# Kernel optimization log

Measured on AMD Instinct MI355X. Metric: run time of the kernel, lower is better.

Reference implementation:

```python
import jax, jax.numpy as jnp
import numpy as np

GRID_LO = 32
GRID_HI = 128
NF = 4          # n_features
K = 9           # num_neighbors
NUM_CLASSES = 36
BS = 128
P_LO = GRID_LO * GRID_LO   # 1024
P_HI = GRID_HI * GRID_HI   # 16384


def _knn_neighbor_indices():
    """Replicates cKDTree(lo_coords).query(hi_coords, k=K)[1]: lo grid has
    spacing ratio=grid_hi//grid_lo, hi grid spacing 1; neighbors sorted by
    distance (stable sort -> ties broken by lower linear index)."""
    ratio = GRID_HI // GRID_LO
    lo = np.stack(np.meshgrid(np.arange(GRID_LO) * ratio,
                              np.arange(GRID_LO) * ratio, indexing='ij'),
                  axis=-1).reshape(-1, 2).astype(np.float64)   # (P_LO, 2)
    hi = np.stack(np.meshgrid(np.arange(GRID_HI),
                              np.arange(GRID_HI), indexing='ij'),
                  axis=-1).reshape(-1, 2).astype(np.float64)   # (P_HI, 2)
    d2 = ((hi[:, None, :] - lo[None, :, :]) ** 2).sum(-1)      # (P_HI, P_LO)
    idx = np.argsort(d2, axis=1, kind='stable')[:, :K]          # (P_HI, K)
    return jnp.asarray(idx, dtype=jnp.int32)


def setup_inputs() -> dict:
    key = jax.random.key(0)
    k1, k2, k3, k4, k5 = jax.random.split(key, 5)
    x = jax.random.normal(k1, (BS, NF * P_LO), dtype=jnp.float32)
    cls_ids = jax.random.randint(k2, (BS,), 0, NUM_CLASSES)
    neighbor_indices = _knn_neighbor_indices()                  # (P_HI, K)
    weight_map = jax.random.normal(k3, (NUM_CLASSES, NF, P_HI, K), dtype=jnp.float32) * 0.05
    bias_low = jax.random.normal(k4, (NUM_CLASSES, NF, P_LO), dtype=jnp.float32) * 0.05
    bias_high = jax.random.normal(k5, (NUM_CLASSES, NF, P_HI), dtype=jnp.float32) * 0.05
    return {"x": x, "cls_ids": cls_ids, "neighbor_indices": neighbor_indices,
            "weight_map": weight_map, "bias_low": bias_low, "bias_high": bias_high}


def reference(x, cls_ids, neighbor_indices, weight_map, bias_low, bias_high):
    # x: (BS, NF*P_LO) -> (BS, NF, P_LO)
    y_low = x.reshape(x.shape[0], NF, P_LO)
    y_low_db = y_low - bias_low[cls_ids]                        # (BS, NF, P_LO)
    # gather k=9 lo-res neighbors for every hi-res pixel (all features at once)
    neigh = y_low_db[:, :, neighbor_indices]                    # (BS, NF, P_HI, K)
    weights = weight_map[cls_ids]                               # (BS, NF, P_HI, K)
    out = jnp.einsum('bfpk,bfpk->bfp', neigh, weights)          # weighted sum over k
    out = out + bias_high[cls_ids]                              # (BS, NF, P_HI)
    return out.reshape(x.shape[0], NF, GRID_HI, GRID_HI)
```

## Files before the change

kernel.cpp:

```cpp
#include <hip/hip_runtime.h>

#define BS      128
#define NF      4
#define NC      36
#define P_LO    1024
#define P_HI    16384
#define KNN     9
#define THREADS 256
#define TILE_P  256
#define NTILES  (P_HI / TILE_P)
#define LIST_OFF 64

__global__ __launch_bounds__(128) void build_lists_kernel(
    const int* __restrict__ cls_ids, int* __restrict__ ws)
{
    __shared__ int cnt[NC];
    const int t = threadIdx.x;
    if (t < NC) cnt[t] = 0;
    __syncthreads();
    if (t < BS) {
        int c = cls_ids[t];
        int pos = atomicAdd(&cnt[c], 1);
        ws[LIST_OFF + c * BS + pos] = t;
    }
    __syncthreads();
    if (t < NC) ws[t] = cnt[t];
}

__device__ __forceinline__ void async_cp16(const void* g, void* l) {
    __builtin_amdgcn_global_load_lds(
        (const __attribute__((address_space(1))) void*)g,
        (__attribute__((address_space(3))) void*)l, 16, 0, 0);
}

__global__ __launch_bounds__(THREADS) void rect_up_kernel(
    const float* __restrict__ x,
    const int*   __restrict__ ws,
    const int*   __restrict__ nbr,
    const float* __restrict__ wmap,
    const float* __restrict__ blo,
    const float* __restrict__ bhi,
    float*       __restrict__ out)
{
    __shared__ __align__(16) char smem[2 * TILE_P * KNN * 4];

    const int tile = blockIdx.x % NTILES;
    const int cf   = blockIdx.x / NTILES;
    const int f    = cf % NF;
    const int cls  = cf / NF;

    const int n_b = ws[cls];
    if (n_b == 0) return;

    const int tid   = threadIdx.x;
    const int tbase = tile * TILE_P;
    const int p     = tbase + tid;

    const float4* wsrc = (const float4*)(wmap + ((size_t)(cls * NF + f) * P_HI + tbase) * KNN);
    const float4* isrc = (const float4*)(nbr + (size_t)tbase * KNN);
    float4* wdst = (float4*)smem;
    float4* idst = (float4*)(smem + TILE_P * KNN * 4);
    async_cp16(wsrc + tid,       wdst + tid);
    async_cp16(wsrc + tid + 256, wdst + tid + 256);
    async_cp16(isrc + tid,       idst + tid);
    async_cp16(isrc + tid + 256, idst + tid + 256);
    if (tid < 64) {
        async_cp16(wsrc + 512 + tid, wdst + 512 + tid);
        async_cp16(isrc + 512 + tid, idst + 512 + tid);
    }

    const float* blp = blo + (size_t)(cls * NF + f) * P_LO;
    float blv0 = blp[tid];
    float blv1 = blp[tid + 256];
    float blv2 = blp[tid + 512];
    float blv3 = blp[tid + 768];
    const float bh = bhi[(size_t)(cls * NF + f) * P_HI + p];
    const int* list = ws + LIST_OFF + cls * BS;

    asm volatile("s_waitcnt vmcnt(0)" ::: "memory");
    __syncthreads();

    float w[KNN]; int nb[KNN];
    {
        const float* wrow = (const float*)smem + (size_t)tid * KNN;
        const int*   irow = (const int*)(smem + TILE_P * KNN * 4) + (size_t)tid * KNN;
        #pragma unroll
        for (int k = 0; k < KNN; ++k) { w[k] = wrow[k]; nb[k] = irow[k]; }
    }
    __syncthreads();

    float4* ybuf = (float4*)smem;

    const int R = (n_b + 3) >> 2;
    for (int r = 0; r < R; ++r) {
        const int s0 = 4 * r;
        const int b0 = list[s0];
        const int b1 = list[(s0 + 1 < n_b) ? s0 + 1 : n_b - 1];
        const int b2 = list[(s0 + 2 < n_b) ? s0 + 2 : n_b - 1];
        const int b3 = list[(s0 + 3 < n_b) ? s0 + 3 : n_b - 1];
        const float* x0 = x + ((size_t)(b0 * NF + f)) * P_LO;
        const float* x1 = x + ((size_t)(b1 * NF + f)) * P_LO;
        const float* x2 = x + ((size_t)(b2 * NF + f)) * P_LO;
        const float* x3 = x + ((size_t)(b3 * NF + f)) * P_LO;

        if (r) __syncthreads();

        {
            float blv[4] = {blv0, blv1, blv2, blv3};
            #pragma unroll
            for (int m = 0; m < 4; ++m) {
                const int q = tid + (m << 8);
                const float bl = blv[m];
                float4 v;
                v.x = x0[q] - bl;
                v.y = x1[q] - bl;
                v.z = x2[q] - bl;
                v.w = x3[q] - bl;
                ybuf[q] = v;
            }
        }
        __syncthreads();

        float a0 = 0.f, a1 = 0.f, a2 = 0.f, a3 = 0.f;
        #pragma unroll
        for (int k = 0; k < KNN; ++k) {
            const float4 yv = ybuf[nb[k]];
            a0 = fmaf(w[k], yv.x, a0);
            a1 = fmaf(w[k], yv.y, a1);
            a2 = fmaf(w[k], yv.z, a2);
            a3 = fmaf(w[k], yv.w, a3);
        }

        out[(size_t)(b0 * NF + f) * P_HI + p] = a0 + bh;
        if (s0 + 1 < n_b) out[(size_t)(b1 * NF + f) * P_HI + p] = a1 + bh;
        if (s0 + 2 < n_b) out[(size_t)(b2 * NF + f) * P_HI + p] = a2 + bh;
        if (s0 + 3 < n_b) out[(size_t)(b3 * NF + f) * P_HI + p] = a3 + bh;
    }
}

extern "C" void kernel_launch(void* const* d_in, const int* in_sizes, int n_in,
                              void* d_out, int out_size, void* d_ws, size_t ws_size,
                              hipStream_t stream) {
    const float* x    = (const float*)d_in[0];
    const int*   cls  = (const int*)d_in[1];
    const int*   nbr  = (const int*)d_in[2];
    const float* wmap = (const float*)d_in[3];
    const float* blo  = (const float*)d_in[4];
    const float* bhi  = (const float*)d_in[5];
    float*       out  = (float*)d_out;
    int*         wsl  = (int*)d_ws;

    build_lists_kernel<<<1, 128, 0, stream>>>(cls, wsl);
    rect_up_kernel<<<NC * NF * NTILES, THREADS, 0, stream>>>(
        x, wsl, nbr, wmap, blo, bhi, out);
}
```

Baseline: 158.1 us.

## Loop features inside each block, prefetch next feature weights, schedule heavy classes first

Each block now handles all four features for one class and tile instead of one feature, so the neighbor-index tile is loaded once and reused across features. The next feature's weights and first x rows are prefetched asynchronously while the current feature computes. The list-building kernel also sorts classes by batch count so that blocks for the most populated classes launch first, reducing tail imbalance. This cuts the grid by a factor of four and raises per-block serial work, and it also increases register use for the prefetched x values.

```diff
diff --git a/kernel.cpp b/kernel.cpp
--- a/kernel.cpp
+++ b/kernel.cpp
@@ -10,13 +10,19 @@
 #define TILE_P  256
 #define NTILES  (P_HI / TILE_P)
 #define LIST_OFF 64
+#define SCHED_OFF 36
+
+#define WBUF_BYTES (TILE_P * KNN * 4)
+#define YBUF_BYTES (P_LO * 16)
 
 __global__ __launch_bounds__(128) void build_lists_kernel(
     const int* __restrict__ cls_ids, int* __restrict__ ws)
 {
     __shared__ int cnt[NC];
+    __shared__ int pk[9];
     const int t = threadIdx.x;
     if (t < NC) cnt[t] = 0;
+    if (t >= 64 && t < 73) pk[t - 64] = 0;
     __syncthreads();
     if (t < BS) {
         int c = cls_ids[t];
@@ -24,7 +30,18 @@
         ws[LIST_OFF + c * BS + pos] = t;
     }
     __syncthreads();
-    if (t < NC) ws[t] = cnt[t];
+    if (t < NC) {
+        int ct = cnt[t];
+        ws[t] = ct;
+        int r = 0;
+        for (int j = 0; j < NC; ++j) {
+            int cj = cnt[j];
+            r += (cj > ct) || (cj == ct && j < t);
+        }
+        atomicOr(&pk[r >> 2], t << ((r & 3) << 3));
+    }
+    __syncthreads();
+    if (t < 9) ws[SCHED_OFF + t] = pk[t];
 }
 
 __device__ __forceinline__ void async_cp16(const void* g, void* l) {
@@ -42,12 +59,11 @@
     const float* __restrict__ bhi,
     float*       __restrict__ out)
 {
-    __shared__ __align__(16) char smem[2 * TILE_P * KNN * 4];
-
-    const int tile = blockIdx.x % NTILES;
-    const int cf   = blockIdx.x / NTILES;
-    const int f    = cf % NF;
-    const int cls  = cf / NF;
+    __shared__ __align__(16) char smem[WBUF_BYTES + YBUF_BYTES];
+
+    const int tile = blockIdx.x & (NTILES - 1);
+    const int g    = blockIdx.x >> 6;
+    const int cls  = (ws[SCHED_OFF + (g >> 2)] >> ((g & 3) << 3)) & 0xFF;
 
     const int n_b = ws[cls];
     if (n_b == 0) return;
@@ -56,85 +72,147 @@
     const int tbase = tile * TILE_P;
     const int p     = tbase + tid;
 
-    const float4* wsrc = (const float4*)(wmap + ((size_t)(cls * NF + f) * P_HI + tbase) * KNN);
-    const float4* isrc = (const float4*)(nbr + (size_t)tbase * KNN);
-    float4* wdst = (float4*)smem;
-    float4* idst = (float4*)(smem + TILE_P * KNN * 4);
-    async_cp16(wsrc + tid,       wdst + tid);
-    async_cp16(wsrc + tid + 256, wdst + tid + 256);
-    async_cp16(isrc + tid,       idst + tid);
-    async_cp16(isrc + tid + 256, idst + tid + 256);
-    if (tid < 64) {
-        async_cp16(wsrc + 512 + tid, wdst + 512 + tid);
-        async_cp16(isrc + 512 + tid, idst + 512 + tid);
-    }
-
-    const float* blp = blo + (size_t)(cls * NF + f) * P_LO;
-    float blv0 = blp[tid];
-    float blv1 = blp[tid + 256];
-    float blv2 = blp[tid + 512];
-    float blv3 = blp[tid + 768];
-    const float bh = bhi[(size_t)(cls * NF + f) * P_HI + p];
+    float4* wbuf  = (float4*)smem;
+    float4* ybuf4 = (float4*)(smem + WBUF_BYTES);
+    float4* idst  = ybuf4;
+
+    {
+        const float4* wsrc = (const float4*)(wmap + ((size_t)(cls * NF + 0) * P_HI + tbase) * KNN);
+        const float4* isrc = (const float4*)(nbr + (size_t)tbase * KNN);
+        async_cp16(wsrc + tid,       wbuf + tid);
+        async_cp16(wsrc + tid + 256, wbuf + tid + 256);
+        async_cp16(isrc + tid,       idst + tid);
+        async_cp16(isrc + tid + 256, idst + tid + 256);
+        if (tid < 64) {
+            async_cp16(wsrc + 512 + tid, wbuf + 512 + tid);
+            async_cp16(isrc + 512 + tid, idst + 512 + tid);
+        }
+    }
+
     const int* list = ws + LIST_OFF + cls * BS;
+    const int bid0 = list[0];
+    const int bid1 = (1 < n_b) ? list[1] : bid0;
+    const int bid2 = (2 < n_b) ? list[2] : bid0;
+    const int bid3 = (3 < n_b) ? list[3] : bid0;
+
+    float xv[16];
+    {
+        const float* x0 = x + ((size_t)(bid0 * NF + 0)) * P_LO;
+        const float* x1 = x + ((size_t)(bid1 * NF + 0)) * P_LO;
+        const float* x2 = x + ((size_t)(bid2 * NF + 0)) * P_LO;
+        const float* x3 = x + ((size_t)(bid3 * NF + 0)) * P_LO;
+        #pragma unroll
+        for (int m = 0; m < 4; ++m) {
+            const int q = tid + (m << 8);
+            xv[m * 4 + 0] = x0[q];
+            xv[m * 4 + 1] = x1[q];
+            xv[m * 4 + 2] = x2[q];
+            xv[m * 4 + 3] = x3[q];
+        }
+    }
 
     asm volatile("s_waitcnt vmcnt(0)" ::: "memory");
     __syncthreads();
 
-    float w[KNN]; int nb[KNN];
+    int nb[KNN];
     {
-        const float* wrow = (const float*)smem + (size_t)tid * KNN;
-        const int*   irow = (const int*)(smem + TILE_P * KNN * 4) + (size_t)tid * KNN;
+        const int* irow = (const int*)(smem + WBUF_BYTES) + (size_t)tid * KNN;
         #pragma unroll
-        for (int k = 0; k < KNN; ++k) { w[k] = wrow[k]; nb[k] = irow[k]; }
-    }
-    __syncthreads();
-
-    float4* ybuf = (float4*)smem;
+        for (int k = 0; k < KNN; ++k) nb[k] = irow[k];
+    }
 
     const int R = (n_b + 3) >> 2;
-    for (int r = 0; r < R; ++r) {
-        const int s0 = 4 * r;
-        const int b0 = list[s0];
-        const int b1 = list[(s0 + 1 < n_b) ? s0 + 1 : n_b - 1];
-        const int b2 = list[(s0 + 2 < n_b) ? s0 + 2 : n_b - 1];
-        const int b3 = list[(s0 + 3 < n_b) ? s0 + 3 : n_b - 1];
-        const float* x0 = x + ((size_t)(b0 * NF + f)) * P_LO;
-        const float* x1 = x + ((size_t)(b1 * NF + f)) * P_LO;
-        const float* x2 = x + ((size_t)(b2 * NF + f)) * P_LO;
-        const float* x3 = x + ((size_t)(b3 * NF + f)) * P_LO;
-
-        if (r) __syncthreads();
-
+
+    for (int f = 0; f < NF; ++f) {
+        float blv[4];
         {
-            float blv[4] = {blv0, blv1, blv2, blv3};
+            const float* blp = blo + (size_t)(cls * NF + f) * P_LO;
             #pragma unroll
-            for (int m = 0; m < 4; ++m) {
-                const int q = tid + (m << 8);
-                const float bl = blv[m];
-                float4 v;
-                v.x = x0[q] - bl;
-                v.y = x1[q] - bl;
-                v.z = x2[q] - bl;
-                v.w = x3[q] - bl;
-                ybuf[q] = v;
+            for (int m = 0; m < 4; ++m) blv[m] = blp[tid + (m << 8)];
+        }
+        const float bh = bhi[(size_t)(cls * NF + f) * P_HI + p];
+
+        float w[KNN];
+        {
+            const float* wrow = (const float*)smem + (size_t)tid * KNN;
+            #pragma unroll
+            for (int k = 0; k < KNN; ++k) w[k] = wrow[k];
+        }
+        __syncthreads();
+
+        for (int r = 0; r < R; ++r) {
+            int c0, c1, c2, c3;
+            if (r == 0) {
+                c0 = bid0; c1 = bid1; c2 = bid2; c3 = bid3;
+                #pragma unroll
+                for (int m = 0; m < 4; ++m) {
+                    float4 v;
+                    v.x = xv[m * 4 + 0] - blv[m];
+                    v.y = xv[m * 4 + 1] - blv[m];
+                    v.z = xv[m * 4 + 2] - blv[m];
+                    v.w = xv[m * 4 + 3] - blv[m];
+                    ybuf4[tid + (m << 8)] = v;
+                }
+            } else {
+                const int s0 = 4 * r;
+                c0 = list[s0];
+                c1 = (s0 + 1 < n_b) ? list[s0 + 1] : c0;
+                c2 = (s0 + 2 < n_b) ? list[s0 + 2] : c0;
+                c3 = (s0 + 3 < n_b) ? list[s0 + 3] : c0;
+                const float* x0 = x + ((size_t)(c0 * NF + f)) * P_LO;
+                const float* x1 = x + ((size_t)(c1 * NF + f)) * P_LO;
+                const float* x2 = x + ((size_t)(c2 * NF + f)) * P_LO;
+                const float* x3 = x + ((size_t)(c3 * NF + f)) * P_LO;
+                #pragma unroll
+                for (int m = 0; m < 4; ++m) {
+                    const int q = tid + (m << 8);
+                    float4 v;
+                    v.x = x0[q] - blv[m];
+                    v.y = x1[q] - blv[m];
+                    v.z = x2[q] - blv[m];
+                    v.w = x3[q] - blv[m];
+                    ybuf4[q] = v;
+                }
             }
-        }
-        __syncthreads();
-
-        float a0 = 0.f, a1 = 0.f, a2 = 0.f, a3 = 0.f;
-        #pragma unroll
-        for (int k = 0; k < KNN; ++k) {
-            const float4 yv = ybuf[nb[k]];
-            a0 = fmaf(w[k], yv.x, a0);
-            a1 = fmaf(w[k], yv.y, a1);
-            a2 = fmaf(w[k], yv.z, a2);
-            a3 = fmaf(w[k], yv.w, a3);
-        }
-
-        out[(size_t)(b0 * NF + f) * P_HI + p] = a0 + bh;
-        if (s0 + 1 < n_b) out[(size_t)(b1 * NF + f) * P_HI + p] = a1 + bh;
-        if (s0 + 2 < n_b) out[(size_t)(b2 * NF + f) * P_HI + p] = a2 + bh;
-        if (s0 + 3 < n_b) out[(size_t)(b3 * NF + f) * P_HI + p] = a3 + bh;
+            __syncthreads();
+
+            if (r == 0 && f + 1 < NF) {
+                const float4* wsrc = (const float4*)(wmap + ((size_t)(cls * NF + f + 1) * P_HI + tbase) * KNN);
+                async_cp16(wsrc + tid,       wbuf + tid);
+                async_cp16(wsrc + tid + 256, wbuf + tid + 256);
+                if (tid < 64) async_cp16(wsrc + 512 + tid, wbuf + 512 + tid);
+                const float* x0 = x + ((size_t)(bid0 * NF + f + 1)) * P_LO;
+                const float* x1 = x + ((size_t)(bid1 * NF + f + 1)) * P_LO;
+                const float* x2 = x + ((size_t)(bid2 * NF + f + 1)) * P_LO;
+                const float* x3 = x + ((size_t)(bid3 * NF + f + 1)) * P_LO;
+                #pragma unroll
+                for (int m = 0; m < 4; ++m) {
+                    const int q = tid + (m << 8);
+                    xv[m * 4 + 0] = x0[q];
+                    xv[m * 4 + 1] = x1[q];
+                    xv[m * 4 + 2] = x2[q];
+                    xv[m * 4 + 3] = x3[q];
+                }
+            }
+
+            float a0 = 0.f, a1 = 0.f, a2 = 0.f, a3 = 0.f;
+            #pragma unroll
+            for (int k = 0; k < KNN; ++k) {
+                const float4 yv = ybuf4[nb[k]];
+                a0 = fmaf(w[k], yv.x, a0);
+                a1 = fmaf(w[k], yv.y, a1);
+                a2 = fmaf(w[k], yv.z, a2);
+                a3 = fmaf(w[k], yv.w, a3);
+            }
+            const int s0 = 4 * r;
+            out[(size_t)(c0 * NF + f) * P_HI + p] = a0 + bh;
+            if (s0 + 1 < n_b) out[(size_t)(c1 * NF + f) * P_HI + p] = a1 + bh;
+            if (s0 + 2 < n_b) out[(size_t)(c2 * NF + f) * P_HI + p] = a2 + bh;
+            if (s0 + 3 < n_b) out[(size_t)(c3 * NF + f) * P_HI + p] = a3 + bh;
+
+            if (r + 1 < R) __syncthreads();
+        }
+        if (f + 1 < NF) __syncthreads();
     }
 }
 
@@ -151,6 +229,6 @@
     int*         wsl  = (int*)d_ws;
 
     build_lists_kernel<<<1, 128, 0, stream>>>(cls, wsl);
-    rect_up_kernel<<<NC * NF * NTILES, THREADS, 0, stream>>>(
+    rect_up_kernel<<<NC * NTILES, THREADS, 0, stream>>>(
         x, wsl, nbr, wmap, blo, bhi, out);
 }
```

New measurement: 163.8 us. 3.6% more time.
